# Kernel tuning notes

Measured on AMD Instinct MI355X. Metric: run time of the kernel, lower is better.

Reference implementation:

```python
import jax, jax.numpy as jnp
import numpy as np

B, S, H = 8, 2048, 1024

def setup_inputs() -> dict:
    key = jax.random.key(0)
    k1, k2, k3, k4, k5, k6 = jax.random.split(key, 6)
    scale = 1.0 / np.sqrt(H)
    return {
        "hidden_states": jax.random.normal(k1, (B, S, H), dtype=jnp.float32),
        "key_padding_mask": jax.random.bernoulli(k2, 0.1, (B, S)),  # True = padded key
        "Wq_w": jax.random.normal(k3, (H, H), dtype=jnp.float32) * scale,
        "Wq_b": jax.random.normal(k4, (H,), dtype=jnp.float32) * 0.01,
        "Wk_w": jax.random.normal(k5, (H, H), dtype=jnp.float32) * scale,
        "Wk_b": jax.random.normal(k6, (H,), dtype=jnp.float32) * 0.01,
    }

def reference(hidden_states, key_padding_mask, Wq_w, Wq_b, Wk_w, Wk_b):
    # torch nn.Linear: y = x @ W.T + b
    q = jnp.einsum("bsh,oh->bso", hidden_states, Wq_w) + Wq_b
    k = jnp.einsum("bsh,oh->bso", hidden_states, Wk_w) + Wk_b
    d = q.shape[-1]
    scores = jnp.einsum("bqd,bkd->bqk", q, k) / jnp.sqrt(jnp.asarray(d, q.dtype))
    # scores[mask] -= inf  -> masked key columns become -inf
    scores = jnp.where(key_padding_mask[:, None, :], -jnp.inf, scores)
    attn = jax.nn.softmax(scores, axis=2)  # [B, S, S]
    out = jnp.einsum("bqk,bkd->bqd", attn, hidden_states)  # values = hidden_states (no proj)
    return out
```

## Files before the change

kernel.cpp:

```cpp
#include <hip/hip_runtime.h>
#include <hip/hip_bf16.h>

using bf16 = __hip_bfloat16;

using frag_ab = __attribute__((ext_vector_type(8))) short;
using frag_cd = __attribute__((ext_vector_type(4))) float;

#define TM 128
#define TN 128
#define TK 32

__device__ __forceinline__ unsigned short f2bu(float f) {
    bf16 h = __float2bfloat16(f);
    return *(unsigned short*)&h;
}

__device__ __forceinline__ void st_c(float* p, float v) { *p = v; }
__device__ __forceinline__ void st_c(bf16* p, float v)  { *p = __float2bfloat16(v); }

__device__ __forceinline__ void load16(const bf16* g, bf16* l) {
    __builtin_amdgcn_global_load_lds(
        (const __attribute__((address_space(1))) unsigned int*)g,
        (__attribute__((address_space(3))) unsigned int*)l,
        16, 0, 0);
}

template <typename TC, bool HAS_BIAS, bool MASK>
__global__ __launch_bounds__(256, 4)
void mfma_gemm_nt(const bf16* __restrict__ A, const bf16* __restrict__ B,
                  const float* __restrict__ bias, const int* __restrict__ mask,
                  TC* __restrict__ C, int N, int K, int lda, int ldb, int ldc,
                  long sA, long sB, long sC, long sM, float scale)
{
    __shared__ bf16 As[2][TM][TK];
    __shared__ bf16 Bs[2][TN][TK];

    const int bz = blockIdx.z;
    const bf16* Ab = A + (long)bz * sA;
    const bf16* Bb = B + (long)bz * sB;
    TC* Cb = C + (long)bz * sC;
    const int* maskb = MASK ? (mask + (long)bz * sM) : nullptr;

    const int t  = threadIdx.x;
    const int m0 = blockIdx.x * TM;
    const int n0 = blockIdx.y * TN;

    const int srow = t >> 2;
    const int c    = t & 3;
    const int gco  = (((c - (srow >> 1)) & 3) << 3);
    const int lco  = c << 3;
    const bf16* ga0 = Ab + (long)(m0 + srow) * lda + gco;
    const bf16* ga1 = ga0 + (long)64 * lda;
    const bf16* gb0 = Bb + (long)(n0 + srow) * ldb + gco;
    const bf16* gb1 = gb0 + (long)64 * ldb;

    const int wave = t >> 6;
    const int lane = t & 63;
    const int wm   = (wave & 1) * 64;
    const int wn   = (wave >> 1) * 64;
    const int lrow = lane & 15;
    const int quad = lane >> 4;
    const int rco  = (((quad + (lrow >> 1)) & 3) << 3);

    frag_cd acc[4][4] = {};

#define STAGE(buf)                                         \
    do {                                                   \
        load16(ga0, &As[buf][srow][lco]);                  \
        load16(ga1, &As[buf][srow + 64][lco]);             \
        load16(gb0, &Bs[buf][srow][lco]);                  \
        load16(gb1, &Bs[buf][srow + 64][lco]);             \
        ga0 += TK; ga1 += TK; gb0 += TK; gb1 += TK;        \
    } while (0)

    STAGE(0);
    __syncthreads();

    int cur = 0;
    for (int k0 = 0; k0 < K; k0 += TK) {
        if (k0 + TK < K) STAGE(cur ^ 1);

        frag_ab af[4], bfv[4];
#pragma unroll
        for (int i = 0; i < 4; ++i)
            af[i] = *(const frag_ab*)&As[cur][wm + i * 16 + lrow][rco];
#pragma unroll
        for (int j = 0; j < 4; ++j)
            bfv[j] = *(const frag_ab*)&Bs[cur][wn + j * 16 + lrow][rco];
#pragma unroll
        for (int i = 0; i < 4; ++i)
#pragma unroll
            for (int j = 0; j < 4; ++j)
                acc[i][j] = __builtin_amdgcn_mfma_f32_16x16x32_bf16(
                    af[i], bfv[j], acc[i][j], 0, 0, 0);

        __syncthreads();
        cur ^= 1;
    }
#undef STAGE

#pragma unroll
    for (int j = 0; j < 4; ++j) {
        const int col = n0 + wn + j * 16 + lrow;
        const float bv = HAS_BIAS ? bias[col] : 0.0f;
        const bool msk = MASK ? (maskb[col] != 0) : false;
#pragma unroll
        for (int i = 0; i < 4; ++i) {
            const int rbase = m0 + wm + i * 16 + quad * 4;
#pragma unroll
            for (int r = 0; r < 4; ++r) {
                float v = acc[i][j][r] * scale + bv;
                if (MASK && msk) v = -INFINITY;
                st_c(&Cb[(long)(rbase + r) * ldc + col], v);
            }
        }
    }
}

__global__ __launch_bounds__(256)
void convert_transpose(const float* __restrict__ X, bf16* __restrict__ Xb,
                       bf16* __restrict__ XT, int S, int H)
{
    __shared__ unsigned short tile[64][72];
    const int b = blockIdx.z;
    const float* Xp = X + (long)b * S * H;
    bf16* Xbp = Xb + (long)b * S * H;
    bf16* XTp = XT + (long)b * H * S;
    const int h0 = blockIdx.x * 64, s0 = blockIdx.y * 64;
    const int t = threadIdx.x;
    const int r  = t >> 4;
    const int c4 = (t & 15) * 4;

#pragma unroll
    for (int p = 0; p < 4; ++p) {
        const int row = r + p * 16;
        const float4 v = *(const float4*)&Xp[(long)(s0 + row) * H + h0 + c4];
        ushort4 u;
        u.x = f2bu(v.x); u.y = f2bu(v.y); u.z = f2bu(v.z); u.w = f2bu(v.w);
        *(ushort4*)&tile[row][c4] = u;
        *(ushort4*)&Xbp[(long)(s0 + row) * H + h0 + c4] = u;
    }
    __syncthreads();
#pragma unroll
    for (int p = 0; p < 4; ++p) {
        const int hrow = r + p * 16;
        ushort4 u;
        u.x = tile[c4 + 0][hrow];
        u.y = tile[c4 + 1][hrow];
        u.z = tile[c4 + 2][hrow];
        u.w = tile[c4 + 3][hrow];
        *(ushort4*)&XTp[(long)(h0 + hrow) * S + s0 + c4] = u;
    }
}

__global__ __launch_bounds__(256)
void convert_w2(const float* __restrict__ wa, const float* __restrict__ wb,
                bf16* __restrict__ out, int n4each)
{
    const int i = blockIdx.x * 256 + threadIdx.x;
    const bool second = i >= n4each;
    const float* src = second ? wb : wa;
    const int j = second ? i - n4each : i;
    const float4 v = ((const float4*)src)[j];
    ushort4 u;
    u.x = f2bu(v.x); u.y = f2bu(v.y); u.z = f2bu(v.z); u.w = f2bu(v.w);
    ((ushort4*)out)[i] = u;
}

__global__ __launch_bounds__(256)
void pack_bias(const float* __restrict__ qb, const float* __restrict__ kb,
               float* __restrict__ out, int H)
{
    const int i = blockIdx.x * 256 + threadIdx.x;
    out[i] = (i < H) ? qb[i] : kb[i - H];
}

__global__ __launch_bounds__(256)
void softmax_kernel(bf16* __restrict__ Smat, int Slen)
{
    const int row = blockIdx.x;
    bf16* srow = Smat + (long)row * Slen;

    const int t    = threadIdx.x;
    const int lane = t & 63;
    const int wid  = t >> 6;

    ushort4 u0 = ((const ushort4*)srow)[t * 2];
    ushort4 u1 = ((const ushort4*)srow)[t * 2 + 1];

    float vals[8];
    {
        const unsigned short us[8] = {u0.x, u0.y, u0.z, u0.w, u1.x, u1.y, u1.z, u1.w};
#pragma unroll
        for (int i = 0; i < 8; ++i) {
            unsigned int w = (unsigned int)us[i] << 16;
            vals[i] = *(float*)&w;
        }
    }

    float mx = vals[0];
#pragma unroll
    for (int i = 1; i < 8; ++i) mx = fmaxf(mx, vals[i]);

    __shared__ float red[4];
#pragma unroll
    for (int o = 32; o > 0; o >>= 1) mx = fmaxf(mx, __shfl_xor(mx, o, 64));
    if (lane == 0) red[wid] = mx;
    __syncthreads();
    mx = fmaxf(fmaxf(red[0], red[1]), fmaxf(red[2], red[3]));
    __syncthreads();

    float sum = 0.0f;
#pragma unroll
    for (int i = 0; i < 8; ++i) {
        const float e = __expf(vals[i] - mx);
        vals[i] = e;
        sum += e;
    }
#pragma unroll
    for (int o = 32; o > 0; o >>= 1) sum += __shfl_xor(sum, o, 64);
    if (lane == 0) red[wid] = sum;
    __syncthreads();
    sum = red[0] + red[1] + red[2] + red[3];

    const float inv = 1.0f / sum;
    ushort4 o0, o1;
    o0.x = f2bu(vals[0] * inv); o0.y = f2bu(vals[1] * inv);
    o0.z = f2bu(vals[2] * inv); o0.w = f2bu(vals[3] * inv);
    o1.x = f2bu(vals[4] * inv); o1.y = f2bu(vals[5] * inv);
    o1.z = f2bu(vals[6] * inv); o1.w = f2bu(vals[7] * inv);
    ((ushort4*)srow)[t * 2]     = o0;
    ((ushort4*)srow)[t * 2 + 1] = o1;
}

extern "C" void kernel_launch(void* const* d_in, const int* in_sizes, int n_in,
                              void* d_out, int out_size, void* d_ws, size_t ws_size,
                              hipStream_t stream)
{
    const float* hidden = (const float*)d_in[0];
    const int*   mask   = (const int*)d_in[1];
    const float* Wq_w   = (const float*)d_in[2];
    const float* Wq_b   = (const float*)d_in[3];
    const float* Wk_w   = (const float*)d_in[4];
    const float* Wk_b   = (const float*)d_in[5];
    float* out = (float*)d_out;

    const int B = 8, S = 2048, H = 1024;
    const int M = B * S;
    const long MH = (long)M * H;

    bf16* QK  = (bf16*)d_ws;
    bf16* XbT = QK + MH * 2;
    bf16* Sb  = XbT + MH;
    bf16* Xb  = Sb;
    bf16* Wb  = Xb + MH;
    float* biasP = (float*)(Wb + 2L * H * H);

    const dim3 blk(256);

    convert_transpose<<<dim3(H / 64, S / 64, B), blk, 0, stream>>>(hidden, Xb, XbT, S, H);
    convert_w2<<<dim3(2 * H * H / 1024), blk, 0, stream>>>(Wq_w, Wk_w, Wb, H * H / 4);
    pack_bias<<<dim3(2 * H / 256), blk, 0, stream>>>(Wq_b, Wk_b, biasP, H);

    mfma_gemm_nt<bf16, true, false><<<dim3(M / TM, 2 * H / TN, 1), blk, 0, stream>>>(
        Xb, Wb, biasP, nullptr, QK, 2 * H, H, H, H, 2 * H, 0, 0, 0, 0, 1.0f);

    mfma_gemm_nt<bf16, false, true><<<dim3(S / TM, S / TN, B), blk, 0, stream>>>(
        QK, QK + H, nullptr, mask, Sb, S, H, 2 * H, 2 * H, S,
        (long)S * 2 * H, (long)S * 2 * H, (long)S * S, S, 1.0f / 32.0f);

    softmax_kernel<<<dim3(B * S), blk, 0, stream>>>(Sb, S);

    mfma_gemm_nt<float, false, false><<<dim3(S / TM, H / TN, B), blk, 0, stream>>>(
        Sb, XbT, nullptr, nullptr, out, H, S, S, S, H,
        (long)S * S, (long)H * S, (long)S * H, 0, 1.0f);
}
```

Measured before the change: 410.7 us.

## Replace GEMM with 256x256-tile, 8-wave, 4-slot pipelined MFMA kernel

Replaces the 128x128, 4-wave, double-buffered GEMM with a 256x256-tile kernel using 8 waves, a 4-slot LDS ring (128 KB) and a phase-interleaved schedule. Each phase issues async global->LDS loads while the MFMAs run, with explicit vmcnt waits, barriers and setprio. It also changes the LDS swizzle. The larger tiles are meant to increase operand reuse and hide memory latency. In exchange, occupancy drops to about one block per CU because of the LDS use, and the grid becomes coarser (e.g. 512 blocks for the batched GEMMs).

New measurement: 413.1 us. About the same (+0.6%).

```diff
diff --git a/kernel.cpp b/kernel.cpp
--- a/kernel.cpp
+++ b/kernel.cpp
@@ -5,10 +5,6 @@
 
 using frag_ab = __attribute__((ext_vector_type(8))) short;
 using frag_cd = __attribute__((ext_vector_type(4))) float;
-
-#define TM 128
-#define TN 128
-#define TK 32
 
 __device__ __forceinline__ unsigned short f2bu(float f) {
     bf16 h = __float2bfloat16(f);
@@ -26,14 +22,13 @@
 }
 
 template <typename TC, bool HAS_BIAS, bool MASK>
-__global__ __launch_bounds__(256, 4)
-void mfma_gemm_nt(const bf16* __restrict__ A, const bf16* __restrict__ B,
-                  const float* __restrict__ bias, const int* __restrict__ mask,
-                  TC* __restrict__ C, int N, int K, int lda, int ldb, int ldc,
-                  long sA, long sB, long sC, long sM, float scale)
-{
-    __shared__ bf16 As[2][TM][TK];
-    __shared__ bf16 Bs[2][TN][TK];
+__global__ __launch_bounds__(512, 2)
+void gemm8p(const bf16* __restrict__ A, const bf16* __restrict__ B,
+            const float* __restrict__ bias, const int* __restrict__ mask,
+            TC* __restrict__ C, int K, int lda, int ldb, int ldc,
+            long sA, long sB, long sC, long sM, float scale)
+{
+    __shared__ short lds[65536];
 
     const int bz = blockIdx.z;
     const bf16* Ab = A + (long)bz * sA;
@@ -41,75 +36,113 @@
     TC* Cb = C + (long)bz * sC;
     const int* maskb = MASK ? (mask + (long)bz * sM) : nullptr;
 
-    const int t  = threadIdx.x;
-    const int m0 = blockIdx.x * TM;
-    const int n0 = blockIdx.y * TN;
-
-    const int srow = t >> 2;
-    const int c    = t & 3;
-    const int gco  = (((c - (srow >> 1)) & 3) << 3);
-    const int lco  = c << 3;
-    const bf16* ga0 = Ab + (long)(m0 + srow) * lda + gco;
-    const bf16* ga1 = ga0 + (long)64 * lda;
-    const bf16* gb0 = Bb + (long)(n0 + srow) * ldb + gco;
-    const bf16* gb1 = gb0 + (long)64 * ldb;
-
-    const int wave = t >> 6;
+    const int t    = threadIdx.x;
+    const int wid  = t >> 6;
     const int lane = t & 63;
-    const int wm   = (wave & 1) * 64;
-    const int wn   = (wave >> 1) * 64;
+    const int m0 = blockIdx.x * 256;
+    const int n0 = blockIdx.y * 256;
+    const int wr = wid >> 2;
+    const int wc = wid & 3;
     const int lrow = lane & 15;
     const int quad = lane >> 4;
-    const int rco  = (((quad + (lrow >> 1)) & 3) << 3);
-
-    frag_cd acc[4][4] = {};
-
-#define STAGE(buf)                                         \
-    do {                                                   \
-        load16(ga0, &As[buf][srow][lco]);                  \
-        load16(ga1, &As[buf][srow + 64][lco]);             \
-        load16(gb0, &Bs[buf][srow][lco]);                  \
-        load16(gb1, &Bs[buf][srow + 64][lco]);             \
-        ga0 += TK; ga1 += TK; gb0 += TK; gb1 += TK;        \
+
+    const int rco   = ((quad ^ (lrow & 3) ^ ((lrow >> 2) & 3)) & 3) * 8;
+    const int a_off = wr * 4096 + lrow * 32 + rco;
+    const int b_off = wc * 2048 + lrow * 32 + rco;
+
+    const int srow = wid * 32 + (lane >> 2);
+    const int gk   = (((lane & 3) ^ ((lane >> 2) & 3) ^ (lane >> 4)) & 3) * 8;
+    const bf16* srcA0 = Ab + (long)(m0 + srow) * lda + gk;
+    const bf16* srcA1 = Ab + (long)(m0 + srow + 16) * lda + gk;
+    const bf16* srcB0 = Bb + (long)(n0 + srow) * ldb + gk;
+    const bf16* srcB1 = Bb + (long)(n0 + srow + 16) * ldb + gk;
+    const int dst0 = wid * 1024 + lane * 8;
+
+    frag_cd acc[8][4] = {};
+
+#define STG(SLOT, PART, K0)                                                     \
+    do {                                                                        \
+        load16((PART ? srcB0 : srcA0) + (K0),                                   \
+               (bf16*)&lds[(SLOT) * 16384 + (PART) * 8192 + dst0]);             \
+        load16((PART ? srcB1 : srcA1) + (K0),                                   \
+               (bf16*)&lds[(SLOT) * 16384 + (PART) * 8192 + dst0 + 512]);       \
     } while (0)
 
-    STAGE(0);
-    __syncthreads();
-
-    int cur = 0;
-    for (int k0 = 0; k0 < K; k0 += TK) {
-        if (k0 + TK < K) STAGE(cur ^ 1);
-
-        frag_ab af[4], bfv[4];
-#pragma unroll
-        for (int i = 0; i < 4; ++i)
-            af[i] = *(const frag_ab*)&As[cur][wm + i * 16 + lrow][rco];
-#pragma unroll
-        for (int j = 0; j < 4; ++j)
-            bfv[j] = *(const frag_ab*)&Bs[cur][wn + j * 16 + lrow][rco];
-#pragma unroll
-        for (int i = 0; i < 4; ++i)
-#pragma unroll
-            for (int j = 0; j < 4; ++j)
-                acc[i][j] = __builtin_amdgcn_mfma_f32_16x16x32_bf16(
-                    af[i], bfv[j], acc[i][j], 0, 0, 0);
-
-        __syncthreads();
-        cur ^= 1;
-    }
-#undef STAGE
+#define PHASE(SLOT, QM, DO_STG, SSLOT, SPART, SK0, VM)                          \
+    do {                                                                        \
+        frag_ab af_[4], bf_[4];                                                 \
+        _Pragma("unroll")                                                       \
+        for (int i_ = 0; i_ < 4; ++i_)                                          \
+            af_[i_] = *(const frag_ab*)&lds[(SLOT) * 16384 + a_off +            \
+                                            (QM) * 2048 + i_ * 512];            \
+        _Pragma("unroll")                                                       \
+        for (int j_ = 0; j_ < 4; ++j_)                                          \
+            bf_[j_] = *(const frag_ab*)&lds[(SLOT) * 16384 + 8192 + b_off +     \
+                                            j_ * 512];                          \
+        if (DO_STG) STG(SSLOT, SPART, SK0);                                     \
+        if ((VM) == 1) asm volatile("s_waitcnt vmcnt(4)" ::: "memory");         \
+        if ((VM) == 2) asm volatile("s_waitcnt vmcnt(0)" ::: "memory");         \
+        __builtin_amdgcn_sched_barrier(0);                                      \
+        __builtin_amdgcn_s_barrier();                                           \
+        asm volatile("s_waitcnt lgkmcnt(0)" ::: "memory");                      \
+        __builtin_amdgcn_sched_barrier(0);                                      \
+        __builtin_amdgcn_s_setprio(1);                                          \
+        _Pragma("unroll")                                                       \
+        for (int i_ = 0; i_ < 4; ++i_)                                          \
+            _Pragma("unroll")                                                   \
+            for (int j_ = 0; j_ < 4; ++j_)                                      \
+                acc[(QM) * 4 + i_][j_] = __builtin_amdgcn_mfma_f32_16x16x32_bf16( \
+                    af_[i_], bf_[j_], acc[(QM) * 4 + i_][j_], 0, 0, 0);         \
+        __builtin_amdgcn_s_setprio(0);                                          \
+        __builtin_amdgcn_sched_barrier(0);                                      \
+        __builtin_amdgcn_s_barrier();                                           \
+    } while (0)
+
+    STG(0, 0, 0);  STG(0, 1, 0);
+    STG(1, 0, 32); STG(1, 1, 32);
+    STG(2, 0, 64); STG(2, 1, 64);
+    asm volatile("s_waitcnt vmcnt(4)" ::: "memory");
+    __builtin_amdgcn_sched_barrier(0);
+    __builtin_amdgcn_s_barrier();
+    __builtin_amdgcn_sched_barrier(0);
+
+    const int NI = K >> 7;
+    for (int it = 0; it < NI - 1; ++it) {
+        const int kb = it << 7;
+        PHASE(0, 0, 1, 3, 0, kb + 96,  0);
+        PHASE(0, 1, 1, 3, 1, kb + 96,  1);
+        PHASE(1, 0, 1, 0, 0, kb + 128, 0);
+        PHASE(1, 1, 1, 0, 1, kb + 128, 0);
+        PHASE(2, 0, 1, 1, 0, kb + 160, 0);
+        PHASE(2, 1, 1, 1, 1, kb + 160, 1);
+        PHASE(3, 0, 1, 2, 0, kb + 192, 0);
+        PHASE(3, 1, 1, 2, 1, kb + 192, 0);
+    }
+    {
+        const int kb = (NI - 1) << 7;
+        PHASE(0, 0, 1, 3, 0, kb + 96, 0);
+        PHASE(0, 1, 1, 3, 1, kb + 96, 1);
+        PHASE(1, 0, 0, 0, 0, 0, 0);
+        PHASE(1, 1, 0, 0, 0, 0, 0);
+        PHASE(2, 0, 0, 0, 0, 0, 0);
+        PHASE(2, 1, 0, 0, 0, 0, 2);
+        PHASE(3, 0, 0, 0, 0, 0, 0);
+        PHASE(3, 1, 0, 0, 0, 0, 0);
+    }
+#undef PHASE
+#undef STG
 
 #pragma unroll
     for (int j = 0; j < 4; ++j) {
-        const int col = n0 + wn + j * 16 + lrow;
+        const int col = n0 + wc * 64 + j * 16 + lrow;
         const float bv = HAS_BIAS ? bias[col] : 0.0f;
         const bool msk = MASK ? (maskb[col] != 0) : false;
 #pragma unroll
-        for (int i = 0; i < 4; ++i) {
-            const int rbase = m0 + wm + i * 16 + quad * 4;
+        for (int ai = 0; ai < 8; ++ai) {
+            const int rbase = m0 + wr * 128 + ai * 16 + quad * 4;
 #pragma unroll
             for (int r = 0; r < 4; ++r) {
-                float v = acc[i][j][r] * scale + bv;
+                float v = acc[ai][j][r] * scale + bv;
                 if (MASK && msk) v = -INFINITY;
                 st_c(&Cb[(long)(rbase + r) * ldc + col], v);
             }
@@ -257,21 +290,22 @@
     float* biasP = (float*)(Wb + 2L * H * H);
 
     const dim3 blk(256);
+    const dim3 blk512(512);
 
     convert_transpose<<<dim3(H / 64, S / 64, B), blk, 0, stream>>>(hidden, Xb, XbT, S, H);
     convert_w2<<<dim3(2 * H * H / 1024), blk, 0, stream>>>(Wq_w, Wk_w, Wb, H * H / 4);
     pack_bias<<<dim3(2 * H / 256), blk, 0, stream>>>(Wq_b, Wk_b, biasP, H);
 
-    mfma_gemm_nt<bf16, true, false><<<dim3(M / TM, 2 * H / TN, 1), blk, 0, stream>>>(
-        Xb, Wb, biasP, nullptr, QK, 2 * H, H, H, H, 2 * H, 0, 0, 0, 0, 1.0f);
-
-    mfma_gemm_nt<bf16, false, true><<<dim3(S / TM, S / TN, B), blk, 0, stream>>>(
-        QK, QK + H, nullptr, mask, Sb, S, H, 2 * H, 2 * H, S,
+    gemm8p<bf16, true, false><<<dim3(M / 256, 2 * H / 256, 1), blk512, 0, stream>>>(
+        Xb, Wb, biasP, nullptr, QK, H, H, H, 2 * H, 0, 0, 0, 0, 1.0f);
+
+    gemm8p<bf16, false, true><<<dim3(S / 256, S / 256, B), blk512, 0, stream>>>(
+        QK, QK + H, nullptr, mask, Sb, H, 2 * H, 2 * H, S,
         (long)S * 2 * H, (long)S * 2 * H, (long)S * S, S, 1.0f / 32.0f);
 
     softmax_kernel<<<dim3(B * S), blk, 0, stream>>>(Sb, S);
 
-    mfma_gemm_nt<float, false, false><<<dim3(S / TM, H / TN, B), blk, 0, stream>>>(
-        Sb, XbT, nullptr, nullptr, out, H, S, S, S, H,
+    gemm8p<float, false, false><<<dim3(S / 256, H / 256, B), blk512, 0, stream>>>(
+        Sb, XbT, nullptr, nullptr, out, S, S, S, H,
         (long)S * S, (long)H * S, (long)S * H, 0, 1.0f);
 }
```
